# Optimization experiments

Hardware: AMD Instinct MI355X
Metric: run time of the kernel (lower is better)

The kernel has to match this reference:

```python
import jax, jax.numpy as jnp
import numpy as np

EPS = 1e-5
TAU = 2.0

# Heaviside spike with spikingjelly's default Sigmoid surrogate gradient (alpha=4)
@jax.custom_vjp
def spike(x):
    return (x >= 0.0).astype(x.dtype)

def _spike_fwd(x):
    return (x >= 0.0).astype(x.dtype), x

def _spike_bwd(x, g):
    a = 4.0
    s = jax.nn.sigmoid(a * x)
    return (g * a * s * (1.0 - s),)

spike.defvjp(_spike_fwd, _spike_bwd)

def lif(x_seq, v_th, v_reset):
    """Multi-step LIF (decay_input=True, detach_reset=True). v_reset=None -> soft reset."""
    def step(v, x):
        if v_reset is None:
            v = v + (x - v) / TAU
        else:
            v = v + (x - (v - v_reset)) / TAU
        s = spike(v - v_th)
        sd = jax.lax.stop_gradient(s)  # detach_reset=True
        if v_reset is None:
            v = v - sd * v_th
        else:
            v = (1.0 - sd) * v + sd * v_reset
        return v, s
    _, s_seq = jax.lax.scan(step, jnp.zeros_like(x_seq[0]), x_seq)
    return s_seq

def conv2d(x, w, groups=1):
    return jax.lax.conv_general_dilated(x, w, (1, 1), 'VALID',
        dimension_numbers=('NCHW', 'OIHW', 'NCHW'), feature_group_count=groups)

def bn(x, p):
    # p: [4, C] = (weight, bias, running_mean, running_var); inference-mode BN
    w, b, m, v = p
    inv = w * jax.lax.rsqrt(v + EPS)
    return x * inv[None, :, None, None] + (b - m * inv)[None, :, None, None]

def bn_pad(x, p):
    # BNAndPadLayer(pad_pixels=1): BN then pad 1px border with the BN of zeros
    y = bn(x, p)
    w, b, m, v = p
    pv = (b - m * w * jax.lax.rsqrt(v + EPS))[None, :, None, None]
    y = jnp.pad(y, ((0, 0), (0, 0), (1, 1), (1, 1)))
    y = y.at[:, :, :1, :].set(pv)
    y = y.at[:, :, -1:, :].set(pv)
    y = y.at[:, :, :, :1].set(pv)
    y = y.at[:, :, :, -1:].set(pv)
    return y

def repconv(x, w1, bn1, dw, pw, bn2):
    y = conv2d(x, w1)                       # 1x1 in->in
    y = bn_pad(y, bn1)                      # BN + 1px pad
    y = conv2d(y, dw, groups=dw.shape[0])   # depthwise 3x3, valid
    y = conv2d(y, pw)                       # 1x1 in->out
    return bn(y, bn2)

def setup_inputs() -> dict:
    T, B, C, H, W = 4, 16, 384, 32, 32
    key = jax.random.key(0)
    ks = iter(jax.random.split(key, 32))
    def bn_params(c):
        k1, k2, k3, k4 = jax.random.split(next(ks), 4)
        return jnp.stack([
            1.0 + 0.1 * jax.random.normal(k1, (c,)),
            0.1 * jax.random.normal(k2, (c,)),
            0.1 * jax.random.normal(k3, (c,)),
            jax.random.uniform(k4, (c,), minval=0.5, maxval=1.5)]).astype(jnp.float32)
    def conv_w(shape, fan_in):
        return (jax.random.normal(next(ks), shape) / np.sqrt(fan_in)).astype(jnp.float32)
    return dict(
        x=jax.random.normal(next(ks), (T, B, C, H, W), dtype=jnp.float32),
        r1_w1=conv_w((C, C, 1, 1), C),
        r1_bn1=bn_params(C),
        r1_dw=conv_w((C, 1, 3, 3), 9),
        r1_pw=conv_w((2 * C, C, 1, 1), C),
        r1_bn2=bn_params(2 * C),
        qkv_bn=bn_params(2 * C),
        r2_w1=conv_w((C, C, 1, 1), C),
        r2_bn1=bn_params(C),
        r2_dw=conv_w((C, 1, 3, 3), 9),
        r2_pw=conv_w((C, C, 1, 1), C),
        r2_bn2=bn_params(C),
        proj_bn=bn_params(C),
        scale=jnp.array([0.1], dtype=jnp.float32),
    )

def reference(x, r1_w1, r1_bn1, r1_dw, r1_pw, r1_bn2, qkv_bn,
              r2_w1, r2_bn1, r2_dw, r2_pw, r2_bn2, proj_bn, scale):
    T, B, C, H, W = x.shape
    xs = lif(x, 1.0, 0.0)                                  # shortcut_lif (hard reset)
    y = repconv(xs.reshape(T * B, C, H, W), r1_w1, r1_bn1, r1_dw, r1_pw, r1_bn2)
    y = bn(y, qkv_bn).reshape(T, B, 2 * C, H, W)           # qkv_conv outer BN
    qk, v = y[:, :, :C], y[:, :, C:]
    qk = lif(qk, 1.0, None)                                # qk_lif (soft reset)
    qk = qk.sum(axis=(-1, -2), keepdims=True)              # jit_sum over H,W -> [T,B,C,1,1]
    qk = lif(qk, 0.5, 0.0)                                 # talking_heads_lif (th=0.5, hard)
    v = lif(v, 1.0, None)                                  # v_lif (soft reset)
    out = qk * v                                           # jit_mul broadcast over H,W
    out = repconv(out.reshape(T * B, C, H, W), r2_w1, r2_bn1, r2_dw, r2_pw, r2_bn2)
    out = bn(out, proj_bn).reshape(T, B, C, H, W)          # proj_conv outer BN
    out = lif(out, 1.0, None)                              # proj_lif (soft reset)
    return out * scale
```

## Files before the change

kernel.cpp:

```cpp
#include <hip/hip_runtime.h>

typedef _Float16 f16;
typedef __attribute__((ext_vector_type(8))) _Float16 f16x8;
typedef __attribute__((ext_vector_type(4))) _Float16 f16x4;
typedef __attribute__((ext_vector_type(4))) float f32x4;

#define TT 4
#define BB 16
#define CC 384

#define SWZ(R) ((((R) & 31)) ^ ((((R) & 4)) << 2))

__device__ __forceinline__ float lif_soft(float x, float& v) {
  v = __fadd_rn(v, __fmul_rn(__fsub_rn(x, v), 0.5f));
  float s = (__fsub_rn(v, 1.0f) >= 0.0f) ? 1.0f : 0.0f;
  v = __fsub_rn(v, s);
  return s;
}
__device__ __forceinline__ float lif_hard(float x, float& v, float vth) {
  v = __fadd_rn(v, __fmul_rn(__fsub_rn(x, v), 0.5f));
  float s = (__fsub_rn(v, vth) >= 0.0f) ? 1.0f : 0.0f;
  if (s != 0.0f) v = 0.0f;
  return s;
}

__global__ __launch_bounds__(256) void k_prep_all(const float* __restrict__ w1, const float* __restrict__ pw,
    const float* __restrict__ q1, const float* __restrict__ qp,
    f16* __restrict__ w1a, f16* __restrict__ w1b, f16* __restrict__ pwa, f16* __restrict__ pwb,
    f16* __restrict__ q1a, f16* __restrict__ q1b, f16* __restrict__ qpa, f16* __restrict__ qpb,
    const float* __restrict__ bn1, const float* __restrict__ bn2, const float* __restrict__ qkv,
    const float* __restrict__ rbn1, const float* __restrict__ rbn2, const float* __restrict__ proj,
    float* __restrict__ par) {
  int bid = blockIdx.x;
  if (bid < 2880) {
    int i = bid*256 + threadIdx.x;
    const float* s; f16 *da, *db; int idx;
    if (i < 147456)      { s = w1; da = w1a; db = w1b; idx = i; }
    else if (i < 442368) { s = pw; da = pwa; db = pwb; idx = i - 147456; }
    else if (i < 589824) { s = q1; da = q1a; db = q1b; idx = i - 442368; }
    else                 { s = qp; da = qpa; db = qpb; idx = i - 589824; }
    float x = s[idx];
    f16 a = (f16)x;
    da[idx] = a;
    db[idx] = (f16)((x - (float)a) * 2048.0f);
    return;
  }
  int c = (bid - 2880)*256 + threadIdx.x;
  float* s1 = par;          float* o1 = par + 384;
  float* sA = par + 768;    float* oA = par + 1536;
  float* s2 = par + 2304;   float* o2 = par + 2688;
  float* sB = par + 3072;   float* oB = par + 3456;
  if (c < 384) {
    double a = (double)bn1[c] / sqrt((double)bn1[3*384+c] + 1e-5);
    s1[c] = (float)a;
    o1[c] = (float)((double)bn1[384+c] - (double)bn1[2*384+c]*a);
    double a2 = (double)rbn1[c] / sqrt((double)rbn1[3*384+c] + 1e-5);
    s2[c] = (float)a2;
    o2[c] = (float)((double)rbn1[384+c] - (double)rbn1[2*384+c]*a2);
    double a3 = (double)rbn2[c] / sqrt((double)rbn2[3*384+c] + 1e-5);
    double b3 = (double)rbn2[384+c] - (double)rbn2[2*384+c]*a3;
    double a4 = (double)proj[c] / sqrt((double)proj[3*384+c] + 1e-5);
    double b4 = (double)proj[384+c] - (double)proj[2*384+c]*a4;
    sB[c] = (float)(a3*a4);
    oB[c] = (float)(b3*a4 + b4);
  }
  if (c < 768) {
    double a5 = (double)bn2[c] / sqrt((double)bn2[3*768+c] + 1e-5);
    double b5 = (double)bn2[768+c] - (double)bn2[2*768+c]*a5;
    double a6 = (double)qkv[c] / sqrt((double)qkv[3*768+c] + 1e-5);
    double b6 = (double)qkv[768+c] - (double)qkv[2*768+c]*a6;
    sA[c] = (float)(a5*a6);
    oA[c] = (float)(b5*a6 + b6);
  }
}

__global__ __launch_bounds__(256) void k_lif_in(const float* __restrict__ x, f16* __restrict__ xs) {
  __shared__ float tile[64][65];
  const int p0 = blockIdx.x * 64, c0 = blockIdx.y * 64, b = blockIdx.z;
  const int l = threadIdx.x & 63, q = threadIdx.x >> 6;
  float v[16];
  #pragma unroll
  for (int j = 0; j < 16; ++j) v[j] = 0.0f;
  for (int t = 0; t < TT; ++t) {
    __syncthreads();
    #pragma unroll
    for (int j = 0; j < 16; ++j) {
      int ci = q + j*4;
      tile[ci][l] = x[(((size_t)(t*BB + b)*CC + c0 + ci) << 10) + p0 + l];
    }
    __syncthreads();
    #pragma unroll
    for (int j = 0; j < 16; ++j) {
      int pi = q + j*4;
      float s = lif_hard(tile[l][pi], v[j], 1.0f);
      xs[((size_t)(t*BB + b)*1024 + p0 + pi)*CC + c0 + l] = (f16)s;
    }
  }
}

__device__ __forceinline__ int fragoff(int row, int fq) {
  return row*64 + ((fq*16) ^ (((row >> 1) & 3) << 4));
}

#define GLL(srcP, dstP) __builtin_amdgcn_global_load_lds( \
    (const __attribute__((address_space(1))) void*)(srcP), \
    (__attribute__((address_space(3))) void*)(dstP), 16, 0, 0)

template<int GATE>
__global__ __launch_bounds__(256, 2) void k_gemmA(const f16* __restrict__ X1,
    const f16* __restrict__ Wa, const f16* __restrict__ Wb,
    const float* __restrict__ scale, const float* __restrict__ bias,
    float* __restrict__ out0, const f16* __restrict__ gatep) {
  __shared__ __align__(16) f16 lds[2*3*4096];
  char* lbase = (char*)lds;
  const int gx = gridDim.x;
  const int bid = blockIdx.y * gx + blockIdx.x;
  const int chunk = (gx * gridDim.y) >> 3;
  const int nb = (bid & 7) * chunk + (bid >> 3);
  const int o0 = (nb % gx) * 128;
  const int m0 = (nb / gx) * 128;
  const int lane = threadIdx.x & 63, wid = threadIdx.x >> 6;
  const int wr = wid >> 1, wc = wid & 1;
  const int fr = lane & 15, fq = lane >> 4;
  f32x4 acc_h[4][4], acc_l[4][4];
  #pragma unroll
  for (int i = 0; i < 4; ++i)
    #pragma unroll
    for (int j = 0; j < 4; ++j) { acc_h[i][j] = (f32x4){0,0,0,0}; acc_l[i][j] = (f32x4){0,0,0,0}; }

  const f16* gp; int i0, nst, arr, row0;
  if (wid == 0)      { gp = X1; arr = 0; i0 = 0; nst = 4; row0 = m0; }
  else if (wid == 1) { gp = X1; arr = 0; i0 = 4; nst = 4; row0 = m0; }
  else if (wid == 2) { gp = Wa; arr = 1; i0 = 0; nst = 8; row0 = o0; }
  else               { gp = Wb; arr = 2; i0 = 0; nst = 8; row0 = o0; }
  const char* srcp[8]; int dsto[8];
  #pragma unroll
  for (int j = 0; j < 8; ++j) {
    int i = i0 + (j < nst ? j : 0);
    int loff = i*1024 + lane*16;
    int row = loff >> 6, col = loff & 63;
    int scol = col ^ (((row >> 1) & 3) << 4);
    srcp[j] = (const char*)gp + (size_t)(row0 + row)*768 + scol;
    dsto[j] = arr*8192 + i*1024;
  }
  int offA[4], offB1[4], offB2[4];
  #pragma unroll
  for (int mi = 0; mi < 4; ++mi) offA[mi] = fragoff(wr*64 + mi*16 + fr, fq);
  #pragma unroll
  for (int oi = 0; oi < 4; ++oi) {
    int o = fragoff(wc*64 + oi*16 + fr, fq);
    offB1[oi] = 8192 + o;
    offB2[oi] = 16384 + o;
  }

  const char* gb = nullptr; f16x8 gcur{}, gnxt{};
  if constexpr (GATE) {
    gb = (const char*)gatep + (size_t)(m0 >> 10)*768 + fq*16;
    gcur = *(const f16x8*)gb; gb += 64;
  }

#define ISSUE_A(BUF) { _Pragma("unroll") for (int j = 0; j < 8; ++j) if (j < nst) { \
    GLL(srcp[j], lbase + (BUF) + dsto[j]); srcp[j] += 64; } }
#define COMPUTE_A(BUF) { f16x8 a1[4], b1[4], b2[4]; \
    _Pragma("unroll") for (int mi = 0; mi < 4; ++mi) { \
      a1[mi] = *(const f16x8*)(lbase + (BUF) + offA[mi]); \
      if constexpr (GATE) a1[mi] = a1[mi] * gcur; } \
    _Pragma("unroll") for (int oi = 0; oi < 4; ++oi) { \
      b1[oi] = *(const f16x8*)(lbase + (BUF) + offB1[oi]); \
      b2[oi] = *(const f16x8*)(lbase + (BUF) + offB2[oi]); } \
    _Pragma("unroll") for (int mi = 0; mi < 4; ++mi) \
      _Pragma("unroll") for (int oi = 0; oi < 4; ++oi) { \
        acc_h[mi][oi] = __builtin_amdgcn_mfma_f32_16x16x32_f16(a1[mi], b1[oi], acc_h[mi][oi], 0, 0, 0); \
        acc_l[mi][oi] = __builtin_amdgcn_mfma_f32_16x16x32_f16(a1[mi], b2[oi], acc_l[mi][oi], 0, 0, 0); } }

  ISSUE_A(0);
  __syncthreads();
  #pragma unroll 1
  for (int it2 = 0; it2 < 6; ++it2) {
    ISSUE_A(24576);
    if constexpr (GATE) { gnxt = *(const f16x8*)gb; gb += 64; }
    COMPUTE_A(0);
    if constexpr (GATE) gcur = gnxt;
    __syncthreads();
    if (it2 < 5) {
      ISSUE_A(0);
      if constexpr (GATE) { gnxt = *(const f16x8*)gb; gb += 64; }
    }
    COMPUTE_A(24576);
    if constexpr (GATE) gcur = gnxt;
    __syncthreads();
  }
#undef ISSUE_A
#undef COMPUTE_A

  #pragma unroll
  for (int oi = 0; oi < 4; ++oi) {
    int o = o0 + wc*64 + oi*16 + fr;
    float sc = scale[o], bi = bias[o];
    #pragma unroll
    for (int mi = 0; mi < 4; ++mi) {
      f32x4 h = acc_h[mi][oi], lo2 = acc_l[mi][oi];
      #pragma unroll
      for (int r = 0; r < 4; ++r) {
        int m = m0 + wr*64 + mi*16 + fq*4 + r;
        float y = fmaf(0.00048828125f, lo2[r], h[r]);
        out0[(size_t)m*384 + o] = fmaf(y, sc, bi);
      }
    }
  }
}

template<int EPI>
__global__ __launch_bounds__(256, 2) void k_gemmB(const f16* __restrict__ X1, const f16* __restrict__ X2,
    const f16* __restrict__ Wa, const f16* __restrict__ Wb,
    const float* __restrict__ scale, const float* __restrict__ bias,
    float* __restrict__ outF, const float* __restrict__ gscale,
    f16* __restrict__ sOut, f16* __restrict__ part) {
  __shared__ __align__(16) f16 lds[32768];
  char* lbase = (char*)lds;
  const int gx = gridDim.x;
  const int bid = blockIdx.y * gx + blockIdx.x;
  const int chunk = (gx * gridDim.y) >> 3;
  const int nb = (bid & 7) * chunk + (bid >> 3);
  const int o0 = (nb % gx) * 128;
  const int mb = nb / gx;
  const int b_ = mb >> 5, p0 = (mb & 31) << 5;
  const int lane = threadIdx.x & 63, wid = threadIdx.x >> 6;
  const int wr = wid >> 1, wc = wid & 1;
  const int fr = lane & 15, fq = lane >> 4;
  f32x4 acc_h[4][4], acc_l[4][4];
  #pragma unroll
  for (int i = 0; i < 4; ++i)
    #pragma unroll
    for (int j = 0; j < 4; ++j) { acc_h[i][j] = (f32x4){0,0,0,0}; acc_l[i][j] = (f32x4){0,0,0,0}; }

  const char* srcp[6]; int dsto[6];
  #pragma unroll
  for (int j = 0; j < 6; ++j) {
    int s = wid*6 + j, arr = s >> 3, inst = s & 7;
    int loff = inst*1024 + lane*16;
    int row = loff >> 6, col = loff & 63;
    int scol = col ^ (((row >> 1) & 3) << 4);
    const f16* gp = (arr == 0) ? X1 : (arr == 1) ? Wa : Wb;
    int gm = (arr == 0) ? (((row >> 5) << 14) + (b_ << 10) + p0 + (row & 31)) : (o0 + row);
    srcp[j] = (const char*)gp + (size_t)gm*768 + scol;
    dsto[j] = arr*8192 + inst*1024;
  }
  const char* a2p[4];
  #pragma unroll
  for (int mi = 0; mi < 4; ++mi) {
    int R = wr*64 + mi*16 + fr;
    int gm2 = ((R >> 5) << 14) + (b_ << 10) + p0 + (R & 31);
    a2p[mi] = (const char*)X2 + (size_t)gm2*768 + fq*16;
  }
  int offA[4], offB1[4], offB2[4];
  #pragma unroll
  for (int mi = 0; mi < 4; ++mi) offA[mi] = fragoff(wr*64 + mi*16 + fr, fq);
  #pragma unroll
  for (int oi = 0; oi < 4; ++oi) {
    int o = fragoff(wc*64 + oi*16 + fr, fq);
    offB1[oi] = 8192 + o;
    offB2[oi] = 16384 + o;
  }

  f16x8 a2c[4], a2n[4];

#define ISSUE_B(BUF) { _Pragma("unroll") for (int j = 0; j < 6; ++j) { \
    GLL(srcp[j], lbase + (BUF) + dsto[j]); srcp[j] += 64; } }
#define LOADA2N { _Pragma("unroll") for (int mi = 0; mi < 4; ++mi) { \
    a2n[mi] = *(const f16x8*)a2p[mi]; a2p[mi] += 64; } }
#define COMPUTE_B(BUF) { f16x8 a1[4], b1[4], b2[4]; \
    _Pragma("unroll") for (int mi = 0; mi < 4; ++mi) \
      a1[mi] = *(const f16x8*)(lbase + (BUF) + offA[mi]); \
    _Pragma("unroll") for (int oi = 0; oi < 4; ++oi) { \
      b1[oi] = *(const f16x8*)(lbase + (BUF) + offB1[oi]); \
      b2[oi] = *(const f16x8*)(lbase + (BUF) + offB2[oi]); } \
    _Pragma("unroll") for (int mi = 0; mi < 4; ++mi) \
      _Pragma("unroll") for (int oi = 0; oi < 4; ++oi) { \
        acc_h[mi][oi] = __builtin_amdgcn_mfma_f32_16x16x32_f16(a1[mi], b1[oi], acc_h[mi][oi], 0, 0, 0); \
        acc_l[mi][oi] = __builtin_amdgcn_mfma_f32_16x16x32_f16(a1[mi], b2[oi], acc_l[mi][oi], 0, 0, 0); \
        acc_l[mi][oi] = __builtin_amdgcn_mfma_f32_16x16x32_f16(a2c[mi], b1[oi], acc_l[mi][oi], 0, 0, 0); } }

  ISSUE_B(0);
  #pragma unroll
  for (int mi = 0; mi < 4; ++mi) { a2c[mi] = *(const f16x8*)a2p[mi]; a2p[mi] += 64; }
  __syncthreads();
  #pragma unroll 1
  for (int it2 = 0; it2 < 6; ++it2) {
    ISSUE_B(24576);
    LOADA2N;
    COMPUTE_B(0);
    #pragma unroll
    for (int mi = 0; mi < 4; ++mi) a2c[mi] = a2n[mi];
    __syncthreads();
    if (it2 < 5) {
      ISSUE_B(0);
      LOADA2N;
    }
    COMPUTE_B(24576);
    #pragma unroll
    for (int mi = 0; mi < 4; ++mi) a2c[mi] = a2n[mi];
    __syncthreads();
  }
#undef ISSUE_B
#undef LOADA2N
#undef COMPUTE_B

  float* T = (float*)lds;
  #pragma unroll
  for (int oi = 0; oi < 4; ++oi) {
    int ol = wc*64 + oi*16 + fr;
    float sc = scale[o0 + ol], bi = bias[o0 + ol];
    #pragma unroll
    for (int mi = 0; mi < 4; ++mi) {
      f32x4 h = acc_h[mi][oi], lo2 = acc_l[mi][oi];
      #pragma unroll
      for (int r = 0; r < 4; ++r) {
        int R = wr*64 + mi*16 + fq*4 + r;
        float y = fmaf(0.00048828125f, lo2[r], h[r]);
        T[R*128 + (ol ^ SWZ(R))] = fmaf(y, sc, bi);
      }
    }
  }
  __syncthreads();
  const int tid = threadIdx.x;
  if constexpr (EPI == 1) {
    const int oc = tid & 127, ph = tid >> 7;
    if (o0 >= 384) {
      const int ocg = (o0 - 384) + oc;
      #pragma unroll
      for (int i = 0; i < 16; ++i) {
        int p = ph*16 + i;
        float v = 0.0f;
        #pragma unroll
        for (int t = 0; t < TT; ++t) {
          int R = t*32 + p;
          float s = lif_soft(T[R*128 + (oc ^ SWZ(R))], v);
          sOut[((size_t)((t*16 + b_)*1024 + p0 + p))*384 + ocg] = (f16)s;
        }
      }
    } else {
      float ps4[4] = {0,0,0,0};
      for (int i = 0; i < 16; ++i) {
        int p = ph*16 + i;
        float v = 0.0f;
        #pragma unroll
        for (int t = 0; t < TT; ++t) {
          int R = t*32 + p;
          ps4[t] += lif_soft(T[R*128 + (oc ^ SWZ(R))], v);
        }
      }
      int slice = (p0 >> 4) + ph;
      #pragma unroll
      for (int t = 0; t < TT; ++t)
        part[(((size_t)slice*4 + t)*16 + b_)*384 + o0 + oc] = (f16)ps4[t];
    }
  } else {
    const int p = tid & 31, cg = tid >> 5;
    const float gsc = gscale[0];
    #pragma unroll
    for (int j = 0; j < 16; ++j) {
      int c = cg*16 + j;
      float v = 0.0f;
      #pragma unroll
      for (int t = 0; t < TT; ++t) {
        int R = t*32 + p;
        float s = lif_soft(T[R*128 + (c ^ SWZ(R))], v) * gsc;
        outF[(((size_t)(t*16 + b_)*384) + o0 + c)*1024 + p0 + p] = s;
      }
    }
  }
}

__global__ __launch_bounds__(256) void k_dw(const float* __restrict__ in, const float* __restrict__ wd,
                                            const float* __restrict__ pv,
                                            f16* __restrict__ outA, f16* __restrict__ outB) {
  const int ct = blockIdx.x, h = blockIdx.y, n = blockIdx.z;
  const int cq = threadIdx.x & 15, wg = threadIdx.x >> 4;
  const int c0 = ct*64 + cq*4;
  const int w0 = wg*2;
  float w9[9][4];
  #pragma unroll
  for (int j = 0; j < 4; ++j)
    #pragma unroll
    for (int k = 0; k < 9; ++k) w9[k][j] = wd[(c0 + j)*9 + k];
  const float4 pv4 = *(const float4*)&pv[c0];
  const float* base = in + (size_t)n*1024*CC;
  float4 col[3][4];
  #pragma unroll
  for (int r = 0; r < 3; ++r)
    #pragma unroll
    for (int j = 0; j < 4; ++j) {
      int hh = h - 1 + r, ww = w0 - 1 + j;
      col[r][j] = ((unsigned)hh < 32u && (unsigned)ww < 32u)
                  ? *(const float4*)&base[(size_t)(hh*32 + ww)*CC + c0] : pv4;
    }
  #pragma unroll
  for (int wi = 0; wi < 2; ++wi) {
    float acc[4] = {0.f, 0.f, 0.f, 0.f};
    #pragma unroll
    for (int dh = 0; dh < 3; ++dh)
      #pragma unroll
      for (int dwj = 0; dwj < 3; ++dwj) {
        float4 vv = col[dh][wi + dwj];
        const float* wk = w9[dh*3 + dwj];
        acc[0] = fmaf(wk[0], vv.x, acc[0]);
        acc[1] = fmaf(wk[1], vv.y, acc[1]);
        acc[2] = fmaf(wk[2], vv.z, acc[2]);
        acc[3] = fmaf(wk[3], vv.w, acc[3]);
      }
    f16x4 a4, b4;
    #pragma unroll
    for (int j = 0; j < 4; ++j) {
      f16 a = (f16)acc[j];
      a4[j] = a;
      b4[j] = (f16)((acc[j] - (float)a) * 2048.0f);
    }
    size_t off = ((size_t)n*1024 + h*32 + w0 + wi)*CC + c0;
    *(f16x4*)&outA[off] = a4;
    *(f16x4*)&outB[off] = b4;
  }
}

__global__ __launch_bounds__(256) void k_gate(const f16* __restrict__ partial, f16* __restrict__ gate16) {
  int g = blockIdx.x*256 + threadIdx.x;
  int b = g / CC, c = g % CC;
  float sums[4];
  #pragma unroll
  for (int t = 0; t < TT; ++t) {
    float s = 0.0f;
    for (int ps = 0; ps < 64; ++ps) s += (float)partial[(((size_t)ps*4 + t)*BB + b)*CC + c];
    sums[t] = s;
  }
  float v = 0.0f;
  #pragma unroll
  for (int t = 0; t < TT; ++t)
    gate16[((size_t)(t*BB + b))*CC + c] = (f16)lif_hard(sums[t], v, 0.5f);
}

extern "C" void kernel_launch(void* const* d_in, const int* in_sizes, int n_in,
                              void* d_out, int out_size, void* d_ws, size_t ws_size,
                              hipStream_t stream) {
  const float* x      = (const float*)d_in[0];
  const float* r1_w1  = (const float*)d_in[1];
  const float* r1_bn1 = (const float*)d_in[2];
  const float* r1_dw  = (const float*)d_in[3];
  const float* r1_pw  = (const float*)d_in[4];
  const float* r1_bn2 = (const float*)d_in[5];
  const float* qkv_bn = (const float*)d_in[6];
  const float* r2_w1  = (const float*)d_in[7];
  const float* r2_bn1 = (const float*)d_in[8];
  const float* r2_dw  = (const float*)d_in[9];
  const float* r2_pw  = (const float*)d_in[10];
  const float* r2_bn2 = (const float*)d_in[11];
  const float* proj_bn= (const float*)d_in[12];
  const float* scale  = (const float*)d_in[13];

  float* ws = (float*)d_ws;
  const size_t SEG = 12582912;
  float* W0f = ws;
  float* W1  = ws + SEG;
  float* W2f = ws + 3*SEG;
  float* W3f = ws + 4*SEG;
  f16* xs  = (f16*)W0f;
  f16* s16 = (f16*)W0f;
  float* t1 = W1;
  float* t2 = W1;
  f16* p1a = (f16*)W2f;
  f16* p2a = (f16*)W2f;
  f16* p1b = (f16*)W3f;
  f16* p2b = (f16*)W3f;

  f16* wsp = (f16*)(ws + 6*SEG);
  f16* w1a = wsp,              *w1b = wsp + 147456;
  f16* pwa = wsp + 294912,     *pwb = wsp + 589824;
  f16* q1a = wsp + 884736,     *q1b = wsp + 1032192;
  f16* qpa = wsp + 1179648,    *qpb = wsp + 1327104;
  f16* partial = wsp + 1474560;
  f16* gate16  = wsp + 3047424;
  float* par = (float*)(wsp + 3072000);
  float* s1 = par,        *o1 = par + 384;
  float* sA = par + 768,  *oA = par + 1536;
  float* s2 = par + 2304, *o2 = par + 2688;
  float* sB = par + 3072, *oB = par + 3456;

  k_prep_all<<<2883, 256, 0, stream>>>(r1_w1, r1_pw, r2_w1, r2_pw,
                                       w1a, w1b, pwa, pwb, q1a, q1b, qpa, qpb,
                                       r1_bn1, r1_bn2, qkv_bn, r2_bn1, r2_bn2, proj_bn, par);
  k_lif_in<<<dim3(16, 6, 16), 256, 0, stream>>>(x, xs);
  k_gemmA<0><<<dim3(3, 512), 256, 0, stream>>>(xs, w1a, w1b, s1, o1, t1, nullptr);
  k_dw<<<dim3(6, 32, 64), 256, 0, stream>>>(t1, r1_dw, o1, p1a, p1b);
  k_gemmB<1><<<dim3(6, 512), 256, 0, stream>>>(p1a, p1b, pwa, pwb, sA, oA,
                                               nullptr, nullptr, s16, partial);
  k_gate<<<24, 256, 0, stream>>>(partial, gate16);
  k_gemmA<1><<<dim3(3, 512), 256, 0, stream>>>(s16, q1a, q1b, s2, o2, t2, gate16);
  k_dw<<<dim3(6, 32, 64), 256, 0, stream>>>(t2, r2_dw, o2, p2a, p2b);
  k_gemmB<2><<<dim3(3, 512), 256, 0, stream>>>(p2a, p2b, qpa, qpb, sB, oB,
                                               (float*)d_out, scale, nullptr, nullptr);
}
```

Measured before the change: 526.4 us.

## Stage X2 operand through LDS via async loads and raise gemmA occupancy hint

In k_gemmB the second A operand (X2) was read directly from global memory into registers per wave. It now goes through LDS with global_load_lds, like the other operands, using a 4-array double buffer where each wave loads one array. This removes the register-held prefetch and per-lane global loads, but raises LDS use to 64KB per block, which may cut occupancy. Separately, k_gemmA's launch bound rises to 3 blocks per CU, which limits registers per thread.

```diff
diff --git a/kernel.cpp b/kernel.cpp
--- a/kernel.cpp
+++ b/kernel.cpp
@@ -107,7 +107,7 @@
     (__attribute__((address_space(3))) void*)(dstP), 16, 0, 0)
 
 template<int GATE>
-__global__ __launch_bounds__(256, 2) void k_gemmA(const f16* __restrict__ X1,
+__global__ __launch_bounds__(256, 3) void k_gemmA(const f16* __restrict__ X1,
     const f16* __restrict__ Wa, const f16* __restrict__ Wb,
     const float* __restrict__ scale, const float* __restrict__ bias,
     float* __restrict__ out0, const f16* __restrict__ gatep) {
@@ -216,7 +216,7 @@
     const float* __restrict__ scale, const float* __restrict__ bias,
     float* __restrict__ outF, const float* __restrict__ gscale,
     f16* __restrict__ sOut, f16* __restrict__ part) {
-  __shared__ __align__(16) f16 lds[32768];
+  __shared__ __align__(16) f16 lds[2*4*4096];
   char* lbase = (char*)lds;
   const int gx = gridDim.x;
   const int bid = blockIdx.y * gx + blockIdx.x;
@@ -234,44 +234,38 @@
     #pragma unroll
     for (int j = 0; j < 4; ++j) { acc_h[i][j] = (f32x4){0,0,0,0}; acc_l[i][j] = (f32x4){0,0,0,0}; }
 
-  const char* srcp[6]; int dsto[6];
-  #pragma unroll
-  for (int j = 0; j < 6; ++j) {
-    int s = wid*6 + j, arr = s >> 3, inst = s & 7;
-    int loff = inst*1024 + lane*16;
+  const f16* gp = (wid == 0) ? X1 : (wid == 1) ? X2 : (wid == 2) ? Wa : Wb;
+  const bool isX = (wid <= 1);
+  const char* srcp[8]; int dsto[8];
+  #pragma unroll
+  for (int i = 0; i < 8; ++i) {
+    int loff = i*1024 + lane*16;
     int row = loff >> 6, col = loff & 63;
     int scol = col ^ (((row >> 1) & 3) << 4);
-    const f16* gp = (arr == 0) ? X1 : (arr == 1) ? Wa : Wb;
-    int gm = (arr == 0) ? (((row >> 5) << 14) + (b_ << 10) + p0 + (row & 31)) : (o0 + row);
-    srcp[j] = (const char*)gp + (size_t)gm*768 + scol;
-    dsto[j] = arr*8192 + inst*1024;
-  }
-  const char* a2p[4];
+    int gm = isX ? (((row >> 5) << 14) + (b_ << 10) + p0 + (row & 31)) : (o0 + row);
+    srcp[i] = (const char*)gp + (size_t)gm*768 + scol;
+    dsto[i] = wid*8192 + i*1024;
+  }
+  int offA1[4], offA2[4], offB1[4], offB2[4];
   #pragma unroll
   for (int mi = 0; mi < 4; ++mi) {
-    int R = wr*64 + mi*16 + fr;
-    int gm2 = ((R >> 5) << 14) + (b_ << 10) + p0 + (R & 31);
-    a2p[mi] = (const char*)X2 + (size_t)gm2*768 + fq*16;
-  }
-  int offA[4], offB1[4], offB2[4];
-  #pragma unroll
-  for (int mi = 0; mi < 4; ++mi) offA[mi] = fragoff(wr*64 + mi*16 + fr, fq);
+    int o = fragoff(wr*64 + mi*16 + fr, fq);
+    offA1[mi] = o;
+    offA2[mi] = 8192 + o;
+  }
   #pragma unroll
   for (int oi = 0; oi < 4; ++oi) {
     int o = fragoff(wc*64 + oi*16 + fr, fq);
-    offB1[oi] = 8192 + o;
-    offB2[oi] = 16384 + o;
-  }
-
-  f16x8 a2c[4], a2n[4];
-
-#define ISSUE_B(BUF) { _Pragma("unroll") for (int j = 0; j < 6; ++j) { \
-    GLL(srcp[j], lbase + (BUF) + dsto[j]); srcp[j] += 64; } }
-#define LOADA2N { _Pragma("unroll") for (int mi = 0; mi < 4; ++mi) { \
-    a2n[mi] = *(const f16x8*)a2p[mi]; a2p[mi] += 64; } }
-#define COMPUTE_B(BUF) { f16x8 a1[4], b1[4], b2[4]; \
-    _Pragma("unroll") for (int mi = 0; mi < 4; ++mi) \
-      a1[mi] = *(const f16x8*)(lbase + (BUF) + offA[mi]); \
+    offB1[oi] = 16384 + o;
+    offB2[oi] = 24576 + o;
+  }
+
+#define ISSUE_B(BUF) { _Pragma("unroll") for (int i = 0; i < 8; ++i) { \
+    GLL(srcp[i], lbase + (BUF) + dsto[i]); srcp[i] += 64; } }
+#define COMPUTE_B(BUF) { f16x8 a1[4], a2[4], b1[4], b2[4]; \
+    _Pragma("unroll") for (int mi = 0; mi < 4; ++mi) { \
+      a1[mi] = *(const f16x8*)(lbase + (BUF) + offA1[mi]); \
+      a2[mi] = *(const f16x8*)(lbase + (BUF) + offA2[mi]); } \
     _Pragma("unroll") for (int oi = 0; oi < 4; ++oi) { \
       b1[oi] = *(const f16x8*)(lbase + (BUF) + offB1[oi]); \
       b2[oi] = *(const f16x8*)(lbase + (BUF) + offB2[oi]); } \
@@ -279,31 +273,20 @@
       _Pragma("unroll") for (int oi = 0; oi < 4; ++oi) { \
         acc_h[mi][oi] = __builtin_amdgcn_mfma_f32_16x16x32_f16(a1[mi], b1[oi], acc_h[mi][oi], 0, 0, 0); \
         acc_l[mi][oi] = __builtin_amdgcn_mfma_f32_16x16x32_f16(a1[mi], b2[oi], acc_l[mi][oi], 0, 0, 0); \
-        acc_l[mi][oi] = __builtin_amdgcn_mfma_f32_16x16x32_f16(a2c[mi], b1[oi], acc_l[mi][oi], 0, 0, 0); } }
+        acc_l[mi][oi] = __builtin_amdgcn_mfma_f32_16x16x32_f16(a2[mi], b1[oi], acc_l[mi][oi], 0, 0, 0); } }
 
   ISSUE_B(0);
-  #pragma unroll
-  for (int mi = 0; mi < 4; ++mi) { a2c[mi] = *(const f16x8*)a2p[mi]; a2p[mi] += 64; }
   __syncthreads();
   #pragma unroll 1
   for (int it2 = 0; it2 < 6; ++it2) {
-    ISSUE_B(24576);
-    LOADA2N;
+    ISSUE_B(32768);
     COMPUTE_B(0);
-    #pragma unroll
-    for (int mi = 0; mi < 4; ++mi) a2c[mi] = a2n[mi];
-    __syncthreads();
-    if (it2 < 5) {
-      ISSUE_B(0);
-      LOADA2N;
-    }
-    COMPUTE_B(24576);
-    #pragma unroll
-    for (int mi = 0; mi < 4; ++mi) a2c[mi] = a2n[mi];
+    __syncthreads();
+    if (it2 < 5) ISSUE_B(0);
+    COMPUTE_B(32768);
     __syncthreads();
   }
 #undef ISSUE_B
-#undef LOADA2N
 #undef COMPUTE_B
 
   float* T = (float*)lds;
```

New measurement: 808.6 us. +53.6%, slower.
